# Kernel optimization log

Measured on AMD Instinct MI355X. Metric: run time of the kernel, lower is better.

## Reference

```python
import jax, jax.numpy as jnp
import numpy as np

D_ATTN = 64


def setup_inputs() -> dict:
    key = jax.random.key(0)
    ks = jax.random.split(key, 10)
    B, N, D_MODEL = 8, 1024, 512
    s = 0.02
    return {
        "x": jax.random.normal(ks[0], (B, N, D_MODEL), jnp.float32),
        "top": jax.random.normal(ks[1], (B, N, N, 16), jnp.float32),
        "Wq": jax.random.normal(ks[2], (D_MODEL, D_ATTN), jnp.float32) * s,
        "bq": jnp.zeros((D_ATTN,), jnp.float32),
        "Wk": jax.random.normal(ks[3], (D_MODEL, D_ATTN), jnp.float32) * s,
        "bk": jnp.zeros((D_ATTN,), jnp.float32),
        "Wv": jax.random.normal(ks[4], (D_MODEL, D_ATTN), jnp.float32) * s,
        "bv": jnp.zeros((D_ATTN,), jnp.float32),
        "Wt": jax.random.normal(ks[5], (16, 1), jnp.float32) * s,
        "bt": jnp.zeros((1,), jnp.float32),
    }


def reference(x, top, Wq, bq, Wk, bk, Wv, bv, Wt, bt):
    # QKV projections: [B,N,d_model] -> [B,N,d_attn]
    Q = x @ Wq + bq
    K = x @ Wk + bk
    V = x @ Wv + bv
    scale = 1.0 / jnp.sqrt(jnp.asarray(D_ATTN, x.dtype))
    # [B,N,N] attention logits
    logits = jnp.einsum("bnd,bmd->bnm", Q, K) * scale
    # learned topological bias: Linear(16,1) on [B,N,N,16] -> [B,N,N]
    bias = jnp.einsum("bnmf,fo->bnmo", top, Wt)[..., 0] + bt[0]
    score = jax.nn.softmax(logits + bias, axis=-1)
    return jnp.einsum("bnm,bmd->bnd", score, V)
```

## Files before the change

### kernel.cpp

```cpp
#include <hip/hip_runtime.h>
#include <hip/hip_bf16.h>

typedef __attribute__((ext_vector_type(8))) short short8;
typedef __attribute__((ext_vector_type(4))) float f32x4;
typedef unsigned short ushort_t;
typedef unsigned int uint_t;

#define D_MODEL 512
#define D_ATTN  64
#define R1      16

__device__ __forceinline__ ushort_t f2bf(float f) {
    uint_t u = __float_as_uint(f);
    u += 0x7FFFu + ((u >> 16) & 1u);
    return (ushort_t)(u >> 16);
}

__global__ __launch_bounds__(192)
void qkv_proj(const float* __restrict__ x,
              const float* __restrict__ Wq, const float* __restrict__ bq,
              const float* __restrict__ Wk, const float* __restrict__ bk,
              const float* __restrict__ Wv, const float* __restrict__ bv,
              ushort_t* __restrict__ Q, ushort_t* __restrict__ K,
              ushort_t* __restrict__ Vt)
{
    const int wv   = threadIdx.x >> 6;
    const int lane = threadIdx.x & 63;
    const size_t row0 = (size_t)blockIdx.x * R1;
    const float* __restrict__ xb = x + row0 * D_MODEL;
    const float* __restrict__ W  = (wv == 0) ? Wq : ((wv == 1) ? Wk : Wv);

    float acc[R1];
#pragma unroll
    for (int r = 0; r < R1; ++r) acc[r] = 0.0f;

    for (int k = 0; k < D_MODEL; k += 4) {
        float w0 = W[(k + 0) * D_ATTN + lane];
        float w1 = W[(k + 1) * D_ATTN + lane];
        float w2 = W[(k + 2) * D_ATTN + lane];
        float w3 = W[(k + 3) * D_ATTN + lane];
#pragma unroll
        for (int r = 0; r < R1; ++r) {
            float4 xv = *(const float4*)(xb + r * D_MODEL + k);
            acc[r] = fmaf(xv.x, w0, acc[r]);
            acc[r] = fmaf(xv.y, w1, acc[r]);
            acc[r] = fmaf(xv.z, w2, acc[r]);
            acc[r] = fmaf(xv.w, w3, acc[r]);
        }
    }

    if (wv == 0) {
        float bias = bq[lane];
#pragma unroll
        for (int r = 0; r < R1; ++r)
            Q[(row0 + r) * D_ATTN + lane] = f2bf((acc[r] + bias) * 0.125f);
    } else if (wv == 1) {
        float bias = bk[lane];
#pragma unroll
        for (int r = 0; r < R1; ++r)
            K[(row0 + r) * D_ATTN + lane] = f2bf(acc[r] + bias);
    } else {
        float bias = bv[lane];
        uint_t pk[8];
#pragma unroll
        for (int r = 0; r < R1; r += 2)
            pk[r >> 1] = (uint_t)f2bf(acc[r] + bias) |
                         ((uint_t)f2bf(acc[r + 1] + bias) << 16);
        const int bb = (int)(row0 >> 10);
        const int n0 = (int)(row0 & 1023);
        uint4* dst = (uint4*)(Vt + ((size_t)bb * 64 + lane) * 1024 + n0);
        dst[0] = make_uint4(pk[0], pk[1], pk[2], pk[3]);
        dst[1] = make_uint4(pk[4], pk[5], pk[6], pk[7]);
    }
}

__global__ __launch_bounds__(256)
void topo_attn(const float* __restrict__ top, const float* __restrict__ Wt,
               const ushort_t* __restrict__ Q, const ushort_t* __restrict__ K,
               const ushort_t* __restrict__ Vt, float* __restrict__ out)
{
    __shared__ float lds[16384];
    const int tid = threadIdx.x;
    const int b   = blockIdx.x >> 6;
    const int bn0 = blockIdx.x << 4;

    float wt[16];
#pragma unroll
    for (int i = 0; i < 16; ++i) wt[i] = Wt[i];
    const float* __restrict__ topb = top + ((size_t)bn0 << 14);
#pragma unroll 2
    for (int it = 0; it < 64; ++it) {
        int r = it >> 2;
        int m = ((it & 3) << 8) + tid;
        const float4* tp = (const float4*)(topb + (((size_t)r) << 14) + ((size_t)m << 4));
        float4 a = tp[0], b4 = tp[1], c4 = tp[2], d4 = tp[3];
        float s = a.x * wt[0];
        s = fmaf(a.y,  wt[1],  s); s = fmaf(a.z,  wt[2],  s); s = fmaf(a.w,  wt[3],  s);
        s = fmaf(b4.x, wt[4],  s); s = fmaf(b4.y, wt[5],  s); s = fmaf(b4.z, wt[6],  s);
        s = fmaf(b4.w, wt[7],  s); s = fmaf(c4.x, wt[8],  s); s = fmaf(c4.y, wt[9],  s);
        s = fmaf(c4.z, wt[10], s); s = fmaf(c4.w, wt[11], s); s = fmaf(d4.x, wt[12], s);
        s = fmaf(d4.y, wt[13], s); s = fmaf(d4.z, wt[14], s); s = fmaf(d4.w, wt[15], s);
        lds[r * 1024 + m] = s;
    }
    __syncthreads();

    const int l = tid & 63, wv = tid >> 6;
    const int lr = l & 15, lg = l >> 4;
    const short8 a0 = *(const short8*)(Q + ((size_t)(bn0 + lr)) * 64 + 8 * lg);
    const short8 a1 = *(const short8*)(Q + ((size_t)(bn0 + lr)) * 64 + 32 + 8 * lg);
    const ushort_t* __restrict__ Kb = K + ((size_t)b << 16);
#pragma unroll 4
    for (int t16 = 0; t16 < 16; ++t16) {
        int m0 = (wv << 8) + (t16 << 4);
        short8 kb0 = *(const short8*)(Kb + (size_t)(m0 + lr) * 64 + 8 * lg);
        short8 kb1 = *(const short8*)(Kb + (size_t)(m0 + lr) * 64 + 32 + 8 * lg);
        f32x4 acc = {0.f, 0.f, 0.f, 0.f};
        acc = __builtin_amdgcn_mfma_f32_16x16x32_bf16(a0, kb0, acc, 0, 0, 0);
        acc = __builtin_amdgcn_mfma_f32_16x16x32_bf16(a1, kb1, acc, 0, 0, 0);
#pragma unroll
        for (int j = 0; j < 4; ++j)
            lds[(4 * lg + j) * 1024 + m0 + lr] += acc[j];
    }
    __syncthreads();

    {
        const int r = tid >> 4, sseg = tid & 15;
        float4 v4[16];
        const float4* rowp = (const float4*)(lds + r * 1024 + sseg * 64);
#pragma unroll
        for (int i = 0; i < 16; ++i) v4[i] = rowp[i];
        __syncthreads();
        float mx = v4[0].x;
#pragma unroll
        for (int i = 0; i < 16; ++i)
            mx = fmaxf(mx, fmaxf(fmaxf(v4[i].x, v4[i].y), fmaxf(v4[i].z, v4[i].w)));
#pragma unroll
        for (int off = 8; off >= 1; off >>= 1) mx = fmaxf(mx, __shfl_xor(mx, off));
        float sum = 0.f;
#pragma unroll
        for (int i = 0; i < 16; ++i) {
            v4[i].x = __expf(v4[i].x - mx); sum += v4[i].x;
            v4[i].y = __expf(v4[i].y - mx); sum += v4[i].y;
            v4[i].z = __expf(v4[i].z - mx); sum += v4[i].z;
            v4[i].w = __expf(v4[i].w - mx); sum += v4[i].w;
        }
#pragma unroll
        for (int off = 8; off >= 1; off >>= 1) sum += __shfl_xor(sum, off);
        float inv = 1.0f / sum;
        ushort_t* pb = ((ushort_t*)lds) + r * 1024 + sseg * 64;
#pragma unroll
        for (int i = 0; i < 8; ++i) {
            uint_t w0 = (uint_t)f2bf(v4[2*i].x * inv)   | ((uint_t)f2bf(v4[2*i].y * inv)   << 16);
            uint_t w1 = (uint_t)f2bf(v4[2*i].z * inv)   | ((uint_t)f2bf(v4[2*i].w * inv)   << 16);
            uint_t w2 = (uint_t)f2bf(v4[2*i+1].x * inv) | ((uint_t)f2bf(v4[2*i+1].y * inv) << 16);
            uint_t w3 = (uint_t)f2bf(v4[2*i+1].z * inv) | ((uint_t)f2bf(v4[2*i+1].w * inv) << 16);
            ((uint4*)pb)[i] = make_uint4(w0, w1, w2, w3);
        }
    }
    __syncthreads();

    {
        f32x4 o[4] = {{0,0,0,0},{0,0,0,0},{0,0,0,0},{0,0,0,0}};
        const ushort_t* __restrict__ pb = ((const ushort_t*)lds) + lr * 1024;
        const ushort_t* __restrict__ Vb = Vt + ((size_t)b << 16);
#pragma unroll 2
        for (int c = 0; c < 8; ++c) {
            int m0 = (wv << 8) + (c << 5) + 8 * lg;
            short8 pa = *(const short8*)(pb + m0);
#pragma unroll
            for (int dt = 0; dt < 4; ++dt) {
                short8 vb = *(const short8*)(Vb + (size_t)(dt * 16 + lr) * 1024 + m0);
                o[dt] = __builtin_amdgcn_mfma_f32_16x16x32_bf16(pa, vb, o[dt], 0, 0, 0);
            }
        }
        float* lo = lds + 8192 + (wv << 10);
#pragma unroll
        for (int dt = 0; dt < 4; ++dt)
#pragma unroll
            for (int j = 0; j < 4; ++j)
                lo[(4 * lg + j) * 64 + dt * 16 + lr] = o[dt][j];
    }
    __syncthreads();

#pragma unroll
    for (int i = 0; i < 4; ++i) {
        int idx = (i << 8) + tid;
        float s2 = lds[8192 + idx] + lds[8192 + 1024 + idx]
                 + lds[8192 + 2048 + idx] + lds[8192 + 3072 + idx];
        out[((size_t)bn0 << 6) + idx] = s2;
    }
}

extern "C" void kernel_launch(void* const* d_in, const int* in_sizes, int n_in,
                              void* d_out, int out_size, void* d_ws, size_t ws_size,
                              hipStream_t stream) {
    const float* x   = (const float*)d_in[0];
    const float* top = (const float*)d_in[1];
    const float* Wq  = (const float*)d_in[2];
    const float* bq  = (const float*)d_in[3];
    const float* Wk  = (const float*)d_in[4];
    const float* bk  = (const float*)d_in[5];
    const float* Wv  = (const float*)d_in[6];
    const float* bv  = (const float*)d_in[7];
    const float* Wt  = (const float*)d_in[8];
    float* out = (float*)d_out;

    ushort_t* Q  = (ushort_t*)d_ws;
    ushort_t* K  = Q + 8 * 1024 * 64;
    ushort_t* Vt = K + 8 * 1024 * 64;

    qkv_proj<<<512, 192, 0, stream>>>(x, Wq, bq, Wk, bk, Wv, bv, Q, K, Vt);
    topo_attn<<<512, 256, 0, stream>>>(top, Wt, Q, K, Vt, out);
}
```

Before: 189.2 us.

## Move topology bias reduction into first kernel alongside QKV projection

```diff
diff --git a/kernel.cpp b/kernel.cpp
--- a/kernel.cpp
+++ b/kernel.cpp
@@ -8,74 +8,116 @@
 
 #define D_MODEL 512
 #define D_ATTN  64
-#define R1      16
+#define QKV_BLOCKS  1024
+#define BIAS_BLOCKS 2048
 
 __device__ __forceinline__ ushort_t f2bf(float f) {
     uint_t u = __float_as_uint(f);
     u += 0x7FFFu + ((u >> 16) & 1u);
     return (ushort_t)(u >> 16);
 }
-
-__global__ __launch_bounds__(192)
-void qkv_proj(const float* __restrict__ x,
-              const float* __restrict__ Wq, const float* __restrict__ bq,
-              const float* __restrict__ Wk, const float* __restrict__ bk,
-              const float* __restrict__ Wv, const float* __restrict__ bv,
-              ushort_t* __restrict__ Q, ushort_t* __restrict__ K,
-              ushort_t* __restrict__ Vt)
+__device__ __forceinline__ float bf2f(ushort_t h) {
+    return __uint_as_float((uint_t)h << 16);
+}
+
+__global__ __launch_bounds__(256)
+void fused_stage1(const float* __restrict__ x, const float* __restrict__ top,
+                  const float* __restrict__ Wq, const float* __restrict__ bq,
+                  const float* __restrict__ Wk, const float* __restrict__ bk,
+                  const float* __restrict__ Wv, const float* __restrict__ bv,
+                  const float* __restrict__ Wt,
+                  ushort_t* __restrict__ Q, ushort_t* __restrict__ K,
+                  ushort_t* __restrict__ Vt, ushort_t* __restrict__ bias)
 {
-    const int wv   = threadIdx.x >> 6;
-    const int lane = threadIdx.x & 63;
-    const size_t row0 = (size_t)blockIdx.x * R1;
-    const float* __restrict__ xb = x + row0 * D_MODEL;
-    const float* __restrict__ W  = (wv == 0) ? Wq : ((wv == 1) ? Wk : Wv);
-
-    float acc[R1];
-#pragma unroll
-    for (int r = 0; r < R1; ++r) acc[r] = 0.0f;
-
-    for (int k = 0; k < D_MODEL; k += 4) {
-        float w0 = W[(k + 0) * D_ATTN + lane];
-        float w1 = W[(k + 1) * D_ATTN + lane];
-        float w2 = W[(k + 2) * D_ATTN + lane];
-        float w3 = W[(k + 3) * D_ATTN + lane];
-#pragma unroll
-        for (int r = 0; r < R1; ++r) {
-            float4 xv = *(const float4*)(xb + r * D_MODEL + k);
-            acc[r] = fmaf(xv.x, w0, acc[r]);
-            acc[r] = fmaf(xv.y, w1, acc[r]);
-            acc[r] = fmaf(xv.z, w2, acc[r]);
-            acc[r] = fmaf(xv.w, w3, acc[r]);
-        }
-    }
-
-    if (wv == 0) {
-        float bias = bq[lane];
-#pragma unroll
-        for (int r = 0; r < R1; ++r)
-            Q[(row0 + r) * D_ATTN + lane] = f2bf((acc[r] + bias) * 0.125f);
-    } else if (wv == 1) {
-        float bias = bk[lane];
-#pragma unroll
-        for (int r = 0; r < R1; ++r)
-            K[(row0 + r) * D_ATTN + lane] = f2bf(acc[r] + bias);
+    const int tid = threadIdx.x;
+    if (blockIdx.x < QKV_BLOCKS) {
+        const int wv = tid >> 6;
+        if (wv == 3) return;
+        const int lane = tid & 63;
+        const size_t row0 = (size_t)blockIdx.x * 8;
+        const float* xb = x + row0 * D_MODEL;
+        { uintptr_t u = (uintptr_t)xb; asm volatile("" : "+v"(u)); xb = (const float*)u; }
+        const float* __restrict__ W = (wv == 0) ? Wq : ((wv == 1) ? Wk : Wv);
+
+        float acc[8];
+#pragma unroll
+        for (int r = 0; r < 8; ++r) acc[r] = 0.0f;
+
+#pragma unroll 2
+        for (int k = 0; k < D_MODEL; k += 4) {
+            float w0 = W[(k + 0) * D_ATTN + lane];
+            float w1 = W[(k + 1) * D_ATTN + lane];
+            float w2 = W[(k + 2) * D_ATTN + lane];
+            float w3 = W[(k + 3) * D_ATTN + lane];
+            float4 xr[8];
+#pragma unroll
+            for (int r = 0; r < 8; ++r)
+                xr[r] = *(const float4*)(xb + r * D_MODEL + k);
+#pragma unroll
+            for (int r = 0; r < 8; ++r) {
+                acc[r] = fmaf(xr[r].x, w0, acc[r]);
+                acc[r] = fmaf(xr[r].y, w1, acc[r]);
+                acc[r] = fmaf(xr[r].z, w2, acc[r]);
+                acc[r] = fmaf(xr[r].w, w3, acc[r]);
+            }
+        }
+
+        if (wv == 0) {
+            float b0 = bq[lane];
+#pragma unroll
+            for (int r = 0; r < 8; ++r)
+                Q[(row0 + r) * D_ATTN + lane] = f2bf((acc[r] + b0) * 0.125f);
+        } else if (wv == 1) {
+            float b0 = bk[lane];
+#pragma unroll
+            for (int r = 0; r < 8; ++r)
+                K[(row0 + r) * D_ATTN + lane] = f2bf(acc[r] + b0);
+        } else {
+            float b0 = bv[lane];
+            uint_t pk[4];
+#pragma unroll
+            for (int r = 0; r < 8; r += 2)
+                pk[r >> 1] = (uint_t)f2bf(acc[r] + b0) |
+                             ((uint_t)f2bf(acc[r + 1] + b0) << 16);
+            const int bb = (int)(row0 >> 10);
+            const int n0 = (int)(row0 & 1023);
+            *(uint4*)(Vt + ((size_t)bb * 64 + lane) * 1024 + n0) =
+                make_uint4(pk[0], pk[1], pk[2], pk[3]);
+        }
     } else {
-        float bias = bv[lane];
-        uint_t pk[8];
-#pragma unroll
-        for (int r = 0; r < R1; r += 2)
-            pk[r >> 1] = (uint_t)f2bf(acc[r] + bias) |
-                         ((uint_t)f2bf(acc[r + 1] + bias) << 16);
-        const int bb = (int)(row0 >> 10);
-        const int n0 = (int)(row0 & 1023);
-        uint4* dst = (uint4*)(Vt + ((size_t)bb * 64 + lane) * 1024 + n0);
-        dst[0] = make_uint4(pk[0], pk[1], pk[2], pk[3]);
-        dst[1] = make_uint4(pk[4], pk[5], pk[6], pk[7]);
+        const size_t g0 = (size_t)(blockIdx.x - QKV_BLOCKS) * 4;
+        const float* __restrict__ topb = top + (g0 << 14);
+        float wt[16];
+#pragma unroll
+        for (int i = 0; i < 16; ++i) wt[i] = Wt[i];
+        uint_t* __restrict__ ob = (uint_t*)(bias + (g0 << 10));
+
+#pragma unroll 2
+        for (int it = 0; it < 8; ++it) {
+            int r = it >> 1;
+            int m = ((it & 1) << 9) + (tid << 1);
+            const float4* tp = (const float4*)(topb + ((size_t)r << 14) + ((size_t)m << 4));
+            float4 a0 = tp[0], a1 = tp[1], a2 = tp[2], a3 = tp[3];
+            float4 c0 = tp[4], c1 = tp[5], c2 = tp[6], c3 = tp[7];
+            float s0 = a0.x * wt[0];
+            s0 = fmaf(a0.y, wt[1],  s0); s0 = fmaf(a0.z, wt[2],  s0); s0 = fmaf(a0.w, wt[3],  s0);
+            s0 = fmaf(a1.x, wt[4],  s0); s0 = fmaf(a1.y, wt[5],  s0); s0 = fmaf(a1.z, wt[6],  s0);
+            s0 = fmaf(a1.w, wt[7],  s0); s0 = fmaf(a2.x, wt[8],  s0); s0 = fmaf(a2.y, wt[9],  s0);
+            s0 = fmaf(a2.z, wt[10], s0); s0 = fmaf(a2.w, wt[11], s0); s0 = fmaf(a3.x, wt[12], s0);
+            s0 = fmaf(a3.y, wt[13], s0); s0 = fmaf(a3.z, wt[14], s0); s0 = fmaf(a3.w, wt[15], s0);
+            float s1 = c0.x * wt[0];
+            s1 = fmaf(c0.y, wt[1],  s1); s1 = fmaf(c0.z, wt[2],  s1); s1 = fmaf(c0.w, wt[3],  s1);
+            s1 = fmaf(c1.x, wt[4],  s1); s1 = fmaf(c1.y, wt[5],  s1); s1 = fmaf(c1.z, wt[6],  s1);
+            s1 = fmaf(c1.w, wt[7],  s1); s1 = fmaf(c2.x, wt[8],  s1); s1 = fmaf(c2.y, wt[9],  s1);
+            s1 = fmaf(c2.z, wt[10], s1); s1 = fmaf(c2.w, wt[11], s1); s1 = fmaf(c3.x, wt[12], s1);
+            s1 = fmaf(c3.y, wt[13], s1); s1 = fmaf(c3.z, wt[14], s1); s1 = fmaf(c3.w, wt[15], s1);
+            ob[(r << 9) + (m >> 1)] = (uint_t)f2bf(s0) | ((uint_t)f2bf(s1) << 16);
+        }
     }
 }
 
 __global__ __launch_bounds__(256)
-void topo_attn(const float* __restrict__ top, const float* __restrict__ Wt,
+void topo_attn(const ushort_t* __restrict__ bias,
                const ushort_t* __restrict__ Q, const ushort_t* __restrict__ K,
                const ushort_t* __restrict__ Vt, float* __restrict__ out)
 {
@@ -84,23 +126,18 @@
     const int b   = blockIdx.x >> 6;
     const int bn0 = blockIdx.x << 4;
 
-    float wt[16];
-#pragma unroll
-    for (int i = 0; i < 16; ++i) wt[i] = Wt[i];
-    const float* __restrict__ topb = top + ((size_t)bn0 << 14);
-#pragma unroll 2
-    for (int it = 0; it < 64; ++it) {
-        int r = it >> 2;
-        int m = ((it & 3) << 8) + tid;
-        const float4* tp = (const float4*)(topb + (((size_t)r) << 14) + ((size_t)m << 4));
-        float4 a = tp[0], b4 = tp[1], c4 = tp[2], d4 = tp[3];
-        float s = a.x * wt[0];
-        s = fmaf(a.y,  wt[1],  s); s = fmaf(a.z,  wt[2],  s); s = fmaf(a.w,  wt[3],  s);
-        s = fmaf(b4.x, wt[4],  s); s = fmaf(b4.y, wt[5],  s); s = fmaf(b4.z, wt[6],  s);
-        s = fmaf(b4.w, wt[7],  s); s = fmaf(c4.x, wt[8],  s); s = fmaf(c4.y, wt[9],  s);
-        s = fmaf(c4.z, wt[10], s); s = fmaf(c4.w, wt[11], s); s = fmaf(d4.x, wt[12], s);
-        s = fmaf(d4.y, wt[13], s); s = fmaf(d4.z, wt[14], s); s = fmaf(d4.w, wt[15], s);
-        lds[r * 1024 + m] = s;
+    const ushort_t* __restrict__ bb = bias + ((size_t)bn0 << 10);
+#pragma unroll
+    for (int it = 0; it < 8; ++it) {
+        int e0 = (it << 11) + (tid << 3);
+        short8 v = *(const short8*)(bb + e0);
+        f32x4 f0, f1;
+#pragma unroll
+        for (int j = 0; j < 4; ++j) f0[j] = bf2f((ushort_t)v[j]);
+#pragma unroll
+        for (int j = 0; j < 4; ++j) f1[j] = bf2f((ushort_t)v[4 + j]);
+        *(f32x4*)(lds + e0)     = f0;
+        *(f32x4*)(lds + e0 + 4) = f1;
     }
     __syncthreads();
 
@@ -205,10 +242,12 @@
     const float* Wt  = (const float*)d_in[8];
     float* out = (float*)d_out;
 
-    ushort_t* Q  = (ushort_t*)d_ws;
-    ushort_t* K  = Q + 8 * 1024 * 64;
-    ushort_t* Vt = K + 8 * 1024 * 64;
-
-    qkv_proj<<<512, 192, 0, stream>>>(x, Wq, bq, Wk, bk, Wv, bv, Q, K, Vt);
-    topo_attn<<<512, 256, 0, stream>>>(top, Wt, Q, K, Vt, out);
-}
+    ushort_t* Q    = (ushort_t*)d_ws;
+    ushort_t* K    = Q + 8 * 1024 * 64;
+    ushort_t* Vt   = K + 8 * 1024 * 64;
+    ushort_t* bias = Vt + 8 * 1024 * 64;
+
+    fused_stage1<<<QKV_BLOCKS + BIAS_BLOCKS, 256, 0, stream>>>(
+        x, top, Wq, bq, Wk, bk, Wv, bv, Wt, Q, K, Vt, bias);
+    topo_attn<<<512, 256, 0, stream>>>(bias, Q, K, Vt, out);
+}
```

New measurement: 236.2 us. 1.25x slower.

## Coalesce topology-bias loads with nontemporal quad-lane reduction; rebalance QKV projection

Applied to the files above, without the earlier changes.

```diff
diff --git a/kernel.cpp b/kernel.cpp
--- a/kernel.cpp
+++ b/kernel.cpp
@@ -8,103 +8,112 @@
 
 #define D_MODEL 512
 #define D_ATTN  64
-#define R1      16
 
 __device__ __forceinline__ ushort_t f2bf(float f) {
     uint_t u = __float_as_uint(f);
     u += 0x7FFFu + ((u >> 16) & 1u);
     return (ushort_t)(u >> 16);
 }
-
-__global__ __launch_bounds__(192)
-void qkv_proj(const float* __restrict__ x,
-              const float* __restrict__ Wq, const float* __restrict__ bq,
-              const float* __restrict__ Wk, const float* __restrict__ bk,
-              const float* __restrict__ Wv, const float* __restrict__ bv,
-              ushort_t* __restrict__ Q, ushort_t* __restrict__ K,
-              ushort_t* __restrict__ Vt)
+__device__ __forceinline__ f32x4 ntload4(const f32x4* p) {
+    return __builtin_nontemporal_load(p);
+}
+
+__global__ __launch_bounds__(256)
+void qkv_all(const float* __restrict__ x,
+             const float* __restrict__ Wq, const float* __restrict__ bq,
+             const float* __restrict__ Wk, const float* __restrict__ bk,
+             const float* __restrict__ Wv, const float* __restrict__ bv,
+             ushort_t* __restrict__ Q, ushort_t* __restrict__ K,
+             ushort_t* __restrict__ Vt)
 {
-    const int wv   = threadIdx.x >> 6;
-    const int lane = threadIdx.x & 63;
-    const size_t row0 = (size_t)blockIdx.x * R1;
-    const float* __restrict__ xb = x + row0 * D_MODEL;
-    const float* __restrict__ W  = (wv == 0) ? Wq : ((wv == 1) ? Wk : Wv);
-
-    float acc[R1];
-#pragma unroll
-    for (int r = 0; r < R1; ++r) acc[r] = 0.0f;
-
+    const int l = threadIdx.x & 63, w = threadIdx.x >> 6;
+    const size_t bn0 = (size_t)blockIdx.x << 4;
+    const int r0 = w << 2;
+    const float* xb = x + (bn0 + r0) * D_MODEL;
+    { uintptr_t u = (uintptr_t)xb; asm volatile("" : "+v"(u)); xb = (const float*)u; }
+
+    float aq[4] = {0,0,0,0}, ak[4] = {0,0,0,0}, av[4] = {0,0,0,0};
+#pragma unroll 2
     for (int k = 0; k < D_MODEL; k += 4) {
-        float w0 = W[(k + 0) * D_ATTN + lane];
-        float w1 = W[(k + 1) * D_ATTN + lane];
-        float w2 = W[(k + 2) * D_ATTN + lane];
-        float w3 = W[(k + 3) * D_ATTN + lane];
-#pragma unroll
-        for (int r = 0; r < R1; ++r) {
-            float4 xv = *(const float4*)(xb + r * D_MODEL + k);
-            acc[r] = fmaf(xv.x, w0, acc[r]);
-            acc[r] = fmaf(xv.y, w1, acc[r]);
-            acc[r] = fmaf(xv.z, w2, acc[r]);
-            acc[r] = fmaf(xv.w, w3, acc[r]);
-        }
-    }
-
-    if (wv == 0) {
-        float bias = bq[lane];
-#pragma unroll
-        for (int r = 0; r < R1; ++r)
-            Q[(row0 + r) * D_ATTN + lane] = f2bf((acc[r] + bias) * 0.125f);
-    } else if (wv == 1) {
-        float bias = bk[lane];
-#pragma unroll
-        for (int r = 0; r < R1; ++r)
-            K[(row0 + r) * D_ATTN + lane] = f2bf(acc[r] + bias);
-    } else {
-        float bias = bv[lane];
-        uint_t pk[8];
-#pragma unroll
-        for (int r = 0; r < R1; r += 2)
-            pk[r >> 1] = (uint_t)f2bf(acc[r] + bias) |
-                         ((uint_t)f2bf(acc[r + 1] + bias) << 16);
-        const int bb = (int)(row0 >> 10);
-        const int n0 = (int)(row0 & 1023);
-        uint4* dst = (uint4*)(Vt + ((size_t)bb * 64 + lane) * 1024 + n0);
-        dst[0] = make_uint4(pk[0], pk[1], pk[2], pk[3]);
-        dst[1] = make_uint4(pk[4], pk[5], pk[6], pk[7]);
-    }
+        float4 xr[4];
+#pragma unroll
+        for (int r = 0; r < 4; ++r) xr[r] = *(const float4*)(xb + r * D_MODEL + k);
+        float wqv[4], wkv[4], wvv[4];
+#pragma unroll
+        for (int kk = 0; kk < 4; ++kk) {
+            wqv[kk] = Wq[(k + kk) * D_ATTN + l];
+            wkv[kk] = Wk[(k + kk) * D_ATTN + l];
+            wvv[kk] = Wv[(k + kk) * D_ATTN + l];
+        }
+#pragma unroll
+        for (int r = 0; r < 4; ++r) {
+            const float xv[4] = {xr[r].x, xr[r].y, xr[r].z, xr[r].w};
+#pragma unroll
+            for (int kk = 0; kk < 4; ++kk) {
+                aq[r] = fmaf(xv[kk], wqv[kk], aq[r]);
+                ak[r] = fmaf(xv[kk], wkv[kk], ak[r]);
+                av[r] = fmaf(xv[kk], wvv[kk], av[r]);
+            }
+        }
+    }
+    const float bqv = bq[l], bkv = bk[l], bvv = bv[l];
+#pragma unroll
+    for (int r = 0; r < 4; ++r) {
+        Q[(bn0 + r0 + r) * D_ATTN + l] = f2bf((aq[r] + bqv) * 0.125f);
+        K[(bn0 + r0 + r) * D_ATTN + l] = f2bf(ak[r] + bkv);
+    }
+    const int b = (int)(bn0 >> 10), n0loc = (int)(bn0 & 1023);
+    uint2 pv;
+    pv.x = (uint_t)f2bf(av[0] + bvv) | ((uint_t)f2bf(av[1] + bvv) << 16);
+    pv.y = (uint_t)f2bf(av[2] + bvv) | ((uint_t)f2bf(av[3] + bvv) << 16);
+    *(uint2*)(Vt + ((size_t)(b * 64 + l) << 10) + n0loc + r0) = pv;
 }
 
 __global__ __launch_bounds__(256)
-void topo_attn(const float* __restrict__ top, const float* __restrict__ Wt,
-               const ushort_t* __restrict__ Q, const ushort_t* __restrict__ K,
-               const ushort_t* __restrict__ Vt, float* __restrict__ out)
+void topo_attn_f(const float* __restrict__ top, const float* __restrict__ Wt,
+                 const ushort_t* __restrict__ Q, const ushort_t* __restrict__ K,
+                 const ushort_t* __restrict__ Vt, float* __restrict__ out)
 {
     __shared__ float lds[16384];
     const int tid = threadIdx.x;
+    const int l = tid & 63, wv = tid >> 6;
     const int b   = blockIdx.x >> 6;
     const int bn0 = blockIdx.x << 4;
 
-    float wt[16];
-#pragma unroll
-    for (int i = 0; i < 16; ++i) wt[i] = Wt[i];
-    const float* __restrict__ topb = top + ((size_t)bn0 << 14);
+    {
+        const float* __restrict__ topb = top + ((size_t)bn0 << 14);
+        const float4 wq = *(const float4*)(Wt + ((l & 3) << 2));
+#pragma unroll
+        for (int rr = 0; rr < 4; ++rr) {
+            const int rloc = (wv << 2) + rr;
+            const f32x4* gp = (const f32x4*)(topb + ((size_t)rloc << 14));
+            float* ldsrow = lds + (rloc << 10);
 #pragma unroll 2
-    for (int it = 0; it < 64; ++it) {
-        int r = it >> 2;
-        int m = ((it & 3) << 8) + tid;
-        const float4* tp = (const float4*)(topb + (((size_t)r) << 14) + ((size_t)m << 4));
-        float4 a = tp[0], b4 = tp[1], c4 = tp[2], d4 = tp[3];
-        float s = a.x * wt[0];
-        s = fmaf(a.y,  wt[1],  s); s = fmaf(a.z,  wt[2],  s); s = fmaf(a.w,  wt[3],  s);
-        s = fmaf(b4.x, wt[4],  s); s = fmaf(b4.y, wt[5],  s); s = fmaf(b4.z, wt[6],  s);
-        s = fmaf(b4.w, wt[7],  s); s = fmaf(c4.x, wt[8],  s); s = fmaf(c4.y, wt[9],  s);
-        s = fmaf(c4.z, wt[10], s); s = fmaf(c4.w, wt[11], s); s = fmaf(d4.x, wt[12], s);
-        s = fmaf(d4.y, wt[13], s); s = fmaf(d4.z, wt[14], s); s = fmaf(d4.w, wt[15], s);
-        lds[r * 1024 + m] = s;
-    }
-    __syncthreads();
-
-    const int l = tid & 63, wv = tid >> 6;
+            for (int g = 0; g < 16; ++g) {
+                f32x4 v0 = ntload4(gp + (g << 8) + l);
+                f32x4 v1 = ntload4(gp + (g << 8) + 64 + l);
+                f32x4 v2 = ntload4(gp + (g << 8) + 128 + l);
+                f32x4 v3 = ntload4(gp + (g << 8) + 192 + l);
+                float p0 = v0[0] * wq.x; p0 = fmaf(v0[1], wq.y, p0); p0 = fmaf(v0[2], wq.z, p0); p0 = fmaf(v0[3], wq.w, p0);
+                float p1 = v1[0] * wq.x; p1 = fmaf(v1[1], wq.y, p1); p1 = fmaf(v1[2], wq.z, p1); p1 = fmaf(v1[3], wq.w, p1);
+                float p2 = v2[0] * wq.x; p2 = fmaf(v2[1], wq.y, p2); p2 = fmaf(v2[2], wq.z, p2); p2 = fmaf(v2[3], wq.w, p2);
+                float p3 = v3[0] * wq.x; p3 = fmaf(v3[1], wq.y, p3); p3 = fmaf(v3[2], wq.z, p3); p3 = fmaf(v3[3], wq.w, p3);
+                p0 += __shfl_xor(p0, 1); p0 += __shfl_xor(p0, 2);
+                p1 += __shfl_xor(p1, 1); p1 += __shfl_xor(p1, 2);
+                p2 += __shfl_xor(p2, 1); p2 += __shfl_xor(p2, 2);
+                p3 += __shfl_xor(p3, 1); p3 += __shfl_xor(p3, 2);
+                if (!(l & 3)) {
+                    int mb = (g << 6) + (l >> 2);
+                    ldsrow[mb]      = p0;
+                    ldsrow[mb + 16] = p1;
+                    ldsrow[mb + 32] = p2;
+                    ldsrow[mb + 48] = p3;
+                }
+            }
+        }
+    }
+    __syncthreads();
+
     const int lr = l & 15, lg = l >> 4;
     const short8 a0 = *(const short8*)(Q + ((size_t)(bn0 + lr)) * 64 + 8 * lg);
     const short8 a1 = *(const short8*)(Q + ((size_t)(bn0 + lr)) * 64 + 32 + 8 * lg);
@@ -209,6 +218,6 @@
     ushort_t* K  = Q + 8 * 1024 * 64;
     ushort_t* Vt = K + 8 * 1024 * 64;
 
-    qkv_proj<<<512, 192, 0, stream>>>(x, Wq, bq, Wk, bk, Wv, bv, Q, K, Vt);
-    topo_attn<<<512, 256, 0, stream>>>(top, Wt, Q, K, Vt, out);
-}
+    qkv_all<<<512, 256, 0, stream>>>(x, Wq, bq, Wk, bk, Wv, bv, Q, K, Vt);
+    topo_attn_f<<<512, 256, 0, stream>>>(top, Wt, Q, K, Vt, out);
+}
```

Result: faster. 164.5 us (-13.1%).
